# Optimization experiments

Measured on AMD Instinct MI355X. Metric: run time of the kernel, lower is better.

Reference implementation:

```python
import jax, jax.numpy as jnp
import numpy as np

D_MODEL = 512
NHEAD = 8
HEAD_DIM = D_MODEL // NHEAD
A, B = 1024, 16


def setup_inputs() -> dict:
    key = jax.random.key(0)
    ks = jax.random.split(key, 6)
    s = 1.0 / np.sqrt(D_MODEL)
    return {
        "src": jax.random.normal(ks[0], (A, B, D_MODEL), jnp.float32),
        "asset_relation_bias": jax.random.normal(ks[1], (A, A), jnp.float32) * 0.1,
        "Wq": jax.random.normal(ks[2], (D_MODEL, D_MODEL), jnp.float32) * s,
        "bq": jnp.zeros((D_MODEL,), jnp.float32),
        "Wk": jax.random.normal(ks[3], (D_MODEL, D_MODEL), jnp.float32) * s,
        "bk": jnp.zeros((D_MODEL,), jnp.float32),
        "Wv": jax.random.normal(ks[4], (D_MODEL, D_MODEL), jnp.float32) * s,
        "bv": jnp.zeros((D_MODEL,), jnp.float32),
        "Wo": jax.random.normal(ks[5], (D_MODEL, D_MODEL), jnp.float32) * s,
        "bo": jnp.zeros((D_MODEL,), jnp.float32),
    }


def reference(src, asset_relation_bias, Wq, bq, Wk, bk, Wv, bv, Wo, bo):
    # src: [A, B, H]; attention is over the asset dim A.
    scale = HEAD_DIM ** -0.5

    def proj_heads(x, W, b):
        y = x @ W.T + b                      # [A, B, H]  (torch Linear: x @ W.T + b)
        y = y.reshape(A, B, NHEAD, HEAD_DIM)
        return jnp.transpose(y, (1, 2, 0, 3))  # [B, nh, A, hd]

    q = proj_heads(src, Wq, bq)
    k = proj_heads(src, Wk, bk)
    v = proj_heads(src, Wv, bv)

    logits = jnp.einsum("bnad,bnkd->bnak", q, k) * scale  # [B, nh, A, A]
    logits = logits + asset_relation_bias[None, None]     # additive relation bias
    attn = jax.nn.softmax(logits, axis=-1)                # dropout = identity (eval)
    out = jnp.einsum("bnak,bnkd->bnad", attn, v)          # [B, nh, A, hd]
    out = jnp.transpose(out, (2, 0, 1, 3)).reshape(A, B, D_MODEL)
    out = out @ Wo.T + bo
    return out
```

## Files before the change

kernel.cpp:

```cpp
#include <hip/hip_runtime.h>
#include <hip/hip_bf16.h>

#define A_DIM 1024
#define B_DIM 16
#define DM    512
#define NH    8
#define HD    64

#define LDT 72

typedef short s16x8 __attribute__((ext_vector_type(8)));
typedef float f32x4 __attribute__((ext_vector_type(4)));

static __device__ __forceinline__ unsigned short f2b(float f) {
    __hip_bfloat16 h = __float2bfloat16(f);
    unsigned short u;
    __builtin_memcpy(&u, &h, 2);
    return u;
}
static __device__ __forceinline__ uint2 cvt4(float4 v) {
    __hip_bfloat162 lo = __float22bfloat162_rn(make_float2(v.x, v.y));
    __hip_bfloat162 hi = __float22bfloat162_rn(make_float2(v.z, v.w));
    unsigned int ulo, uhi;
    __builtin_memcpy(&ulo, &lo, 4);
    __builtin_memcpy(&uhi, &hi, 4);
    return make_uint2(ulo, uhi);
}

__global__ __launch_bounds__(256) void cvt_src(
    const float* __restrict__ in, short* __restrict__ out)
{
    int i = (blockIdx.x * 256 + threadIdx.x) * 8;
    float4 a = *(const float4*)&in[i];
    float4 b = *(const float4*)&in[i + 4];
    *(uint2*)&out[i]     = cvt4(a);
    *(uint2*)&out[i + 4] = cvt4(b);
}

__global__ __launch_bounds__(256) void cvt_w(
    const float* __restrict__ Wq, const float* __restrict__ Wk,
    const float* __restrict__ Wv, const float* __restrict__ Wo,
    short* __restrict__ Wall)
{
    int i = blockIdx.x * 256 + threadIdx.x;
    int mat = i >> 15;
    const float* W = (mat == 0) ? Wq : (mat == 1) ? Wk : (mat == 2) ? Wv : Wo;
    int j = (i & 32767) * 8;
    float4 a = *(const float4*)&W[j];
    float4 b = *(const float4*)&W[j + 4];
    *(uint2*)&Wall[mat * (DM * DM) + j]     = cvt4(a);
    *(uint2*)&Wall[mat * (DM * DM) + j + 4] = cvt4(b);
}

__global__ __launch_bounds__(256) void qkv_gemm_bf(
    const short* __restrict__ Sb, const short* __restrict__ Wall,
    const float* __restrict__ bq, const float* __restrict__ bk,
    const float* __restrict__ bv,
    short* __restrict__ Qb, short* __restrict__ Kb, short* __restrict__ Vb)
{
    __shared__ short As[128 * LDT];
    __shared__ short Bs[128 * LDT];

    const int tid  = threadIdx.x;
    const int wave = tid >> 6, lane = tid & 63;
    const int quad = lane >> 4, l16 = lane & 15;
    const int waveM = (wave >> 1) * 64, waveN = (wave & 1) * 64;
    const int mbase = blockIdx.y * 128;
    const int nbase = blockIdx.x * 128;
    const int mat   = nbase >> 9;
    const short* Wm   = Wall + mat * (DM * DM);
    const float* bvec = (mat == 0) ? bq : (mat == 1) ? bk : bv;
    short* dst        = (mat == 0) ? Qb : (mat == 1) ? Kb : Vb;
    const float oscale = (mat == 0) ? 0.125f : 1.0f;
    const int wrow0 = nbase & 511;

    f32x4 acc[4][4];
    #pragma unroll
    for (int i = 0; i < 4; i++)
        #pragma unroll
        for (int j = 0; j < 4; j++)
            acc[i][j] = (f32x4){0.f, 0.f, 0.f, 0.f};

    for (int kb = 0; kb < 8; ++kb) {
        __syncthreads();
        #pragma unroll
        for (int p = 0; p < 4; p++) {
            int chunk = tid + p * 256;
            int row = chunk >> 3, c = chunk & 7;
            *(s16x8*)&As[row * LDT + c * 8] =
                *(const s16x8*)&Sb[(mbase + row) * 512 + kb * 64 + c * 8];
            *(s16x8*)&Bs[row * LDT + c * 8] =
                *(const s16x8*)&Wm[(wrow0 + row) * 512 + kb * 64 + c * 8];
        }
        __syncthreads();
        #pragma unroll
        for (int k0i = 0; k0i < 2; k0i++) {
            s16x8 af[4], bf[4];
            #pragma unroll
            for (int mi = 0; mi < 4; mi++)
                af[mi] = *(const s16x8*)&As[(waveM + mi * 16 + l16) * LDT + (k0i * 4 + quad) * 8];
            #pragma unroll
            for (int ni = 0; ni < 4; ni++)
                bf[ni] = *(const s16x8*)&Bs[(waveN + ni * 16 + l16) * LDT + (k0i * 4 + quad) * 8];
            #pragma unroll
            for (int mi = 0; mi < 4; mi++)
                #pragma unroll
                for (int ni = 0; ni < 4; ni++)
                    acc[mi][ni] = __builtin_amdgcn_mfma_f32_16x16x32_bf16(
                        af[mi], bf[ni], acc[mi][ni], 0, 0, 0);
        }
    }

    #pragma unroll
    for (int mi = 0; mi < 4; mi++) {
        #pragma unroll
        for (int ni = 0; ni < 4; ni++) {
            #pragma unroll
            for (int r = 0; r < 4; r++) {
                int t = mbase + waveM + mi * 16 + quad * 4 + r;
                int o = wrow0 + waveN + ni * 16 + l16;
                float v = (acc[mi][ni][r] + bvec[o]) * oscale;
                int a = t >> 4, bb = t & 15, n = o >> 6, d = o & 63;
                dst[((bb * NH + n) * A_DIM + a) * HD + d] = (short)f2b(v);
            }
        }
    }
}

__global__ __launch_bounds__(256) void qkv_gemm(
    const float* __restrict__ src,
    const float* __restrict__ Wq, const float* __restrict__ bq,
    const float* __restrict__ Wk, const float* __restrict__ bk,
    const float* __restrict__ Wv, const float* __restrict__ bv,
    short* __restrict__ Qb, short* __restrict__ Kb, short* __restrict__ Vb)
{
    __shared__ short As[128 * LDT];
    __shared__ short Bs[128 * LDT];

    const int tid  = threadIdx.x;
    const int wave = tid >> 6, lane = tid & 63;
    const int quad = lane >> 4, l16 = lane & 15;
    const int waveM = (wave >> 1) * 64, waveN = (wave & 1) * 64;
    const int mbase = blockIdx.y * 128;
    const int nbase = blockIdx.x * 128;
    const int mat   = nbase >> 9;
    const float* W    = (mat == 0) ? Wq : (mat == 1) ? Wk : Wv;
    const float* bvec = (mat == 0) ? bq : (mat == 1) ? bk : bv;
    short* dst        = (mat == 0) ? Qb : (mat == 1) ? Kb : Vb;
    const float oscale = (mat == 0) ? 0.125f : 1.0f;
    const int wrow0 = nbase & 511;

    f32x4 acc[4][4];
    #pragma unroll
    for (int i = 0; i < 4; i++)
        #pragma unroll
        for (int j = 0; j < 4; j++)
            acc[i][j] = (f32x4){0.f, 0.f, 0.f, 0.f};

    for (int kb = 0; kb < 8; ++kb) {
        __syncthreads();
        #pragma unroll
        for (int p = 0; p < 8; p++) {
            int chunk = tid + p * 256;
            int row = chunk >> 4, c = chunk & 15;
            float4 a4 = *(const float4*)&src[(mbase + row) * 512 + kb * 64 + c * 4];
            *(uint2*)&As[row * LDT + c * 4] = cvt4(a4);
            float4 w4 = *(const float4*)&W[(wrow0 + row) * 512 + kb * 64 + c * 4];
            *(uint2*)&Bs[row * LDT + c * 4] = cvt4(w4);
        }
        __syncthreads();
        #pragma unroll
        for (int k0i = 0; k0i < 2; k0i++) {
            s16x8 af[4], bf[4];
            #pragma unroll
            for (int mi = 0; mi < 4; mi++)
                af[mi] = *(const s16x8*)&As[(waveM + mi * 16 + l16) * LDT + (k0i * 4 + quad) * 8];
            #pragma unroll
            for (int ni = 0; ni < 4; ni++)
                bf[ni] = *(const s16x8*)&Bs[(waveN + ni * 16 + l16) * LDT + (k0i * 4 + quad) * 8];
            #pragma unroll
            for (int mi = 0; mi < 4; mi++)
                #pragma unroll
                for (int ni = 0; ni < 4; ni++)
                    acc[mi][ni] = __builtin_amdgcn_mfma_f32_16x16x32_bf16(
                        af[mi], bf[ni], acc[mi][ni], 0, 0, 0);
        }
    }

    #pragma unroll
    for (int mi = 0; mi < 4; mi++) {
        #pragma unroll
        for (int ni = 0; ni < 4; ni++) {
            #pragma unroll
            for (int r = 0; r < 4; r++) {
                int t = mbase + waveM + mi * 16 + quad * 4 + r;
                int o = wrow0 + waveN + ni * 16 + l16;
                float v = (acc[mi][ni][r] + bvec[o]) * oscale;
                int a = t >> 4, bb = t & 15, n = o >> 6, d = o & 63;
                dst[((bb * NH + n) * A_DIM + a) * HD + d] = (short)f2b(v);
            }
        }
    }
}

__global__ __launch_bounds__(256) void attn_kernel(
    const short* __restrict__ Qb, const short* __restrict__ Kb,
    const short* __restrict__ Vb, const float* __restrict__ bias,
    short* __restrict__ AO)
{
    __shared__ short Ks[64 * LDT];
    __shared__ short Vt[64 * LDT];
    __shared__ short Ps[4][16 * LDT];

    const int tid  = threadIdx.x;
    const int wave = tid >> 6, lane = tid & 63;
    const int quad = lane >> 4, l16 = lane & 15;
    const int bn = blockIdx.y;
    const int qrow0 = blockIdx.x * 64 + wave * 16;

    const short* Qg = Qb + bn * (A_DIM * HD);
    const short* Kg = Kb + bn * (A_DIM * HD);
    const short* Vg = Vb + bn * (A_DIM * HD);

    s16x8 qf[2];
    #pragma unroll
    for (int k0i = 0; k0i < 2; k0i++)
        qf[k0i] = *(const s16x8*)&Qg[(qrow0 + l16) * HD + k0i * 32 + quad * 8];

    float lsum[4];
    f32x4 of[4];
    #pragma unroll
    for (int r = 0; r < 4; r++) lsum[r] = 0.f;
    #pragma unroll
    for (int db = 0; db < 4; db++) of[db] = (f32x4){0.f, 0.f, 0.f, 0.f};

    for (int kb = 0; kb < 16; ++kb) {
        __syncthreads();
        #pragma unroll
        for (int p = 0; p < 2; p++) {
            int chunk = tid + p * 256;
            int row = chunk >> 3, c = chunk & 7;
            *(s16x8*)&Ks[row * LDT + c * 8] =
                *(const s16x8*)&Kg[(kb * 64 + row) * HD + c * 8];
            s16x8 vv = *(const s16x8*)&Vg[(kb * 64 + row) * HD + c * 8];
            #pragma unroll
            for (int j = 0; j < 8; j++) {
                int d = c * 8 + j;
                Vt[d * LDT + (((row >> 3) ^ c) << 3) + (row & 7)] = vv[j];
            }
        }
        __syncthreads();

        float sv[4][4];
        #pragma unroll
        for (int cb = 0; cb < 4; cb++) {
            f32x4 s = (f32x4){0.f, 0.f, 0.f, 0.f};
            #pragma unroll
            for (int k0i = 0; k0i < 2; k0i++) {
                s16x8 kf = *(const s16x8*)&Ks[(cb * 16 + l16) * LDT + (k0i * 4 + quad) * 8];
                s = __builtin_amdgcn_mfma_f32_16x16x32_bf16(qf[k0i], kf, s, 0, 0, 0);
            }
            #pragma unroll
            for (int r = 0; r < 4; r++) {
                int arow = qrow0 + quad * 4 + r;
                int kcol = kb * 64 + cb * 16 + l16;
                sv[cb][r] = s[r] + bias[arow * A_DIM + kcol];
            }
        }

        #pragma unroll
        for (int r = 0; r < 4; r++) {
            int prow = quad * 4 + r;
            #pragma unroll
            for (int cb = 0; cb < 4; cb++) {
                float pv = __expf(sv[cb][r]);
                lsum[r] += pv;
                Ps[wave][prow * LDT + cb * 16 + l16] = (short)f2b(pv);
            }
        }

        #pragma unroll
        for (int k0i = 0; k0i < 2; k0i++) {
            s16x8 pf = *(const s16x8*)&Ps[wave][l16 * LDT + (k0i * 4 + quad) * 8];
            #pragma unroll
            for (int db = 0; db < 4; db++) {
                int rr = db * 16 + l16;
                s16x8 vf = *(const s16x8*)&Vt[rr * LDT +
                            (((k0i * 4 + quad) ^ (rr >> 3)) << 3)];
                of[db] = __builtin_amdgcn_mfma_f32_16x16x32_bf16(pf, vf, of[db], 0, 0, 0);
            }
        }
    }

    #pragma unroll
    for (int r = 0; r < 4; r++) {
        float ps = lsum[r];
        ps += __shfl_xor(ps, 1);
        ps += __shfl_xor(ps, 2);
        ps += __shfl_xor(ps, 4);
        ps += __shfl_xor(ps, 8);
        lsum[r] = 1.0f / ps;
    }

    const int b = bn >> 3, n = bn & 7;
    #pragma unroll
    for (int db = 0; db < 4; db++) {
        #pragma unroll
        for (int r = 0; r < 4; r++) {
            int a = qrow0 + quad * 4 + r;
            int d = db * 16 + l16;
            float v = of[db][r] * lsum[r];
            AO[(a * B_DIM + b) * DM + n * HD + d] = (short)f2b(v);
        }
    }
}

__global__ __launch_bounds__(256) void out_gemm_bf(
    const short* __restrict__ Xin,
    const short* __restrict__ Wob, const float* __restrict__ bo,
    float* __restrict__ out)
{
    __shared__ short As[128 * LDT];
    __shared__ short Bs[128 * LDT];

    const int tid  = threadIdx.x;
    const int wave = tid >> 6, lane = tid & 63;
    const int quad = lane >> 4, l16 = lane & 15;
    const int waveM = (wave >> 1) * 64, waveN = (wave & 1) * 64;
    const int mbase = blockIdx.y * 128;
    const int nbase = blockIdx.x * 128;

    f32x4 acc[4][4];
    #pragma unroll
    for (int i = 0; i < 4; i++)
        #pragma unroll
        for (int j = 0; j < 4; j++)
            acc[i][j] = (f32x4){0.f, 0.f, 0.f, 0.f};

    for (int kb = 0; kb < 8; ++kb) {
        __syncthreads();
        #pragma unroll
        for (int p = 0; p < 4; p++) {
            int chunk = tid + p * 256;
            int row = chunk >> 3, c = chunk & 7;
            *(s16x8*)&As[row * LDT + c * 8] =
                *(const s16x8*)&Xin[(mbase + row) * 512 + kb * 64 + c * 8];
            *(s16x8*)&Bs[row * LDT + c * 8] =
                *(const s16x8*)&Wob[(nbase + row) * 512 + kb * 64 + c * 8];
        }
        __syncthreads();
        #pragma unroll
        for (int k0i = 0; k0i < 2; k0i++) {
            s16x8 af[4], bf[4];
            #pragma unroll
            for (int mi = 0; mi < 4; mi++)
                af[mi] = *(const s16x8*)&As[(waveM + mi * 16 + l16) * LDT + (k0i * 4 + quad) * 8];
            #pragma unroll
            for (int ni = 0; ni < 4; ni++)
                bf[ni] = *(const s16x8*)&Bs[(waveN + ni * 16 + l16) * LDT + (k0i * 4 + quad) * 8];
            #pragma unroll
            for (int mi = 0; mi < 4; mi++)
                #pragma unroll
                for (int ni = 0; ni < 4; ni++)
                    acc[mi][ni] = __builtin_amdgcn_mfma_f32_16x16x32_bf16(
                        af[mi], bf[ni], acc[mi][ni], 0, 0, 0);
        }
    }

    #pragma unroll
    for (int mi = 0; mi < 4; mi++) {
        #pragma unroll
        for (int ni = 0; ni < 4; ni++) {
            #pragma unroll
            for (int r = 0; r < 4; r++) {
                int t = mbase + waveM + mi * 16 + quad * 4 + r;
                int o = nbase + waveN + ni * 16 + l16;
                out[t * 512 + o] = acc[mi][ni][r] + bo[o];
            }
        }
    }
}

__global__ __launch_bounds__(256) void out_gemm(
    const short* __restrict__ Xin,
    const float* __restrict__ Wo, const float* __restrict__ bo,
    float* __restrict__ out)
{
    __shared__ short As[128 * LDT];
    __shared__ short Bs[128 * LDT];

    const int tid  = threadIdx.x;
    const int wave = tid >> 6, lane = tid & 63;
    const int quad = lane >> 4, l16 = lane & 15;
    const int waveM = (wave >> 1) * 64, waveN = (wave & 1) * 64;
    const int mbase = blockIdx.y * 128;
    const int nbase = blockIdx.x * 128;

    f32x4 acc[4][4];
    #pragma unroll
    for (int i = 0; i < 4; i++)
        #pragma unroll
        for (int j = 0; j < 4; j++)
            acc[i][j] = (f32x4){0.f, 0.f, 0.f, 0.f};

    for (int kb = 0; kb < 8; ++kb) {
        __syncthreads();
        #pragma unroll
        for (int p = 0; p < 4; p++) {
            int chunk = tid + p * 256;
            int row = chunk >> 3, c = chunk & 7;
            *(s16x8*)&As[row * LDT + c * 8] =
                *(const s16x8*)&Xin[(mbase + row) * 512 + kb * 64 + c * 8];
        }
        #pragma unroll
        for (int p = 0; p < 8; p++) {
            int chunk = tid + p * 256;
            int row = chunk >> 4, c = chunk & 15;
            float4 w4 = *(const float4*)&Wo[(nbase + row) * 512 + kb * 64 + c * 4];
            *(uint2*)&Bs[row * LDT + c * 4] = cvt4(w4);
        }
        __syncthreads();
        #pragma unroll
        for (int k0i = 0; k0i < 2; k0i++) {
            s16x8 af[4], bf[4];
            #pragma unroll
            for (int mi = 0; mi < 4; mi++)
                af[mi] = *(const s16x8*)&As[(waveM + mi * 16 + l16) * LDT + (k0i * 4 + quad) * 8];
            #pragma unroll
            for (int ni = 0; ni < 4; ni++)
                bf[ni] = *(const s16x8*)&Bs[(waveN + ni * 16 + l16) * LDT + (k0i * 4 + quad) * 8];
            #pragma unroll
            for (int mi = 0; mi < 4; mi++)
                #pragma unroll
                for (int ni = 0; ni < 4; ni++)
                    acc[mi][ni] = __builtin_amdgcn_mfma_f32_16x16x32_bf16(
                        af[mi], bf[ni], acc[mi][ni], 0, 0, 0);
        }
    }

    #pragma unroll
    for (int mi = 0; mi < 4; mi++) {
        #pragma unroll
        for (int ni = 0; ni < 4; ni++) {
            #pragma unroll
            for (int r = 0; r < 4; r++) {
                int t = mbase + waveM + mi * 16 + quad * 4 + r;
                int o = nbase + waveN + ni * 16 + l16;
                out[t * 512 + o] = acc[mi][ni][r] + bo[o];
            }
        }
    }
}

extern "C" void kernel_launch(void* const* d_in, const int* in_sizes, int n_in,
                              void* d_out, int out_size, void* d_ws, size_t ws_size,
                              hipStream_t stream) {
    const float* src  = (const float*)d_in[0];
    const float* bias = (const float*)d_in[1];
    const float* Wq   = (const float*)d_in[2];
    const float* bq   = (const float*)d_in[3];
    const float* Wk   = (const float*)d_in[4];
    const float* bk   = (const float*)d_in[5];
    const float* Wv   = (const float*)d_in[6];
    const float* bv   = (const float*)d_in[7];
    const float* Wo   = (const float*)d_in[8];
    const float* bo   = (const float*)d_in[9];

    short* ws = (short*)d_ws;
    short* Qb = ws;
    short* Kb = ws + (size_t)(1 << 23);
    short* Vb = ws + (size_t)(2 << 23);

    const bool big2   = ws_size >= (size_t)(66u << 20);
    const bool big_ws = ws_size >= (size_t)(64u << 20);

    if (big2) {
        short* Sb   = ws + (size_t)3 * (1 << 23);
        short* Wall = ws + (size_t)4 * (1 << 23);
        short* AO   = Sb;

        cvt_src<<<dim3(4096), 256, 0, stream>>>(src, Sb);
        cvt_w<<<dim3(512), 256, 0, stream>>>(Wq, Wk, Wv, Wo, Wall);
        qkv_gemm_bf<<<dim3(12, 128), 256, 0, stream>>>(Sb, Wall, bq, bk, bv, Qb, Kb, Vb);
        attn_kernel<<<dim3(16, 128), 256, 0, stream>>>(Qb, Kb, Vb, bias, AO);
        out_gemm_bf<<<dim3(4, 128), 256, 0, stream>>>(AO, Wall + 3 * (DM * DM), bo,
                                                      (float*)d_out);
    } else {
        short* AO = big_ws ? (ws + (size_t)3 * (1 << 23))
                           : (short*)d_out;

        qkv_gemm<<<dim3(12, 128), 256, 0, stream>>>(src, Wq, bq, Wk, bk, Wv, bv, Qb, Kb, Vb);
        attn_kernel<<<dim3(16, 128), 256, 0, stream>>>(Qb, Kb, Vb, bias, AO);

        if (big_ws) {
            out_gemm<<<dim3(4, 128), 256, 0, stream>>>(AO, Wo, bo, (float*)d_out);
        } else {
            float* Cs = (float*)d_ws;
            out_gemm<<<dim3(4, 128), 256, 0, stream>>>(AO, Wo, bo, Cs);
            (void)hipMemcpyAsync(d_out, Cs, (size_t)out_size * sizeof(float),
                                 hipMemcpyDeviceToDevice, stream);
        }
    }
}
```

Before: 241.6 us.

## Use direct global-to-LDS loads with XOR-swizzled tiles in projection GEMMs

Replaces the register-staged global-to-shared copies in the QKV and output projection GEMMs with global_load_lds 16-byte direct loads into LDS. The padded LDT=72 layout becomes an unpadded 64-wide tile with an XOR swizzle on the 8-element column chunk, which keeps fragment reads free of bank conflicts. The aim is to cut VGPR traffic and instruction count in the tile-load phase. It depends on the hardware supporting 16-byte LDS-direct loads, and the attention kernel, which likely dominates runtime, is untouched.

Result: no change. 241.8 us (+0.1%).

```diff
diff --git a/kernel.cpp b/kernel.cpp
--- a/kernel.cpp
+++ b/kernel.cpp
@@ -25,6 +25,12 @@
     __builtin_memcpy(&ulo, &lo, 4);
     __builtin_memcpy(&uhi, &hi, 4);
     return make_uint2(ulo, uhi);
+}
+
+static __device__ __forceinline__ void gl_lds16(const short* g, short* l) {
+    __builtin_amdgcn_global_load_lds(
+        (const __attribute__((address_space(1))) unsigned int*)g,
+        (__attribute__((address_space(3))) unsigned int*)l, 16, 0, 0);
 }
 
 __global__ __launch_bounds__(256) void cvt_src(
@@ -58,8 +64,8 @@
     const float* __restrict__ bv,
     short* __restrict__ Qb, short* __restrict__ Kb, short* __restrict__ Vb)
 {
-    __shared__ short As[128 * LDT];
-    __shared__ short Bs[128 * LDT];
+    __shared__ __align__(16) short As[128 * 64];
+    __shared__ __align__(16) short Bs[128 * 64];
 
     const int tid  = threadIdx.x;
     const int wave = tid >> 6, lane = tid & 63;
@@ -74,6 +80,10 @@
     const float oscale = (mat == 0) ? 0.125f : 1.0f;
     const int wrow0 = nbase & 511;
 
+    const int srow = lane >> 3;
+    const int scol = (lane & 7) ^ srow;
+    const int cxa  = l16 & 7;
+
     f32x4 acc[4][4];
     #pragma unroll
     for (int i = 0; i < 4; i++)
@@ -85,12 +95,12 @@
         __syncthreads();
         #pragma unroll
         for (int p = 0; p < 4; p++) {
-            int chunk = tid + p * 256;
-            int row = chunk >> 3, c = chunk & 7;
-            *(s16x8*)&As[row * LDT + c * 8] =
-                *(const s16x8*)&Sb[(mbase + row) * 512 + kb * 64 + c * 8];
-            *(s16x8*)&Bs[row * LDT + c * 8] =
-                *(const s16x8*)&Wm[(wrow0 + row) * 512 + kb * 64 + c * 8];
+            int ch = wave + p * 4;
+            int r  = ch * 8 + srow;
+            gl_lds16(&Sb[(mbase + r) * 512 + kb * 64 + scol * 8],
+                     &As[ch * 8 * 64]);
+            gl_lds16(&Wm[(wrow0 + r) * 512 + kb * 64 + scol * 8],
+                     &Bs[ch * 8 * 64]);
         }
         __syncthreads();
         #pragma unroll
@@ -98,10 +108,12 @@
             s16x8 af[4], bf[4];
             #pragma unroll
             for (int mi = 0; mi < 4; mi++)
-                af[mi] = *(const s16x8*)&As[(waveM + mi * 16 + l16) * LDT + (k0i * 4 + quad) * 8];
+                af[mi] = *(const s16x8*)&As[(waveM + mi * 16 + l16) * 64
+                                            + (((k0i * 4 + quad) ^ cxa) * 8)];
             #pragma unroll
             for (int ni = 0; ni < 4; ni++)
-                bf[ni] = *(const s16x8*)&Bs[(waveN + ni * 16 + l16) * LDT + (k0i * 4 + quad) * 8];
+                bf[ni] = *(const s16x8*)&Bs[(waveN + ni * 16 + l16) * 64
+                                            + (((k0i * 4 + quad) ^ cxa) * 8)];
             #pragma unroll
             for (int mi = 0; mi < 4; mi++)
                 #pragma unroll
@@ -320,8 +332,8 @@
     const short* __restrict__ Wob, const float* __restrict__ bo,
     float* __restrict__ out)
 {
-    __shared__ short As[128 * LDT];
-    __shared__ short Bs[128 * LDT];
+    __shared__ __align__(16) short As[128 * 64];
+    __shared__ __align__(16) short Bs[128 * 64];
 
     const int tid  = threadIdx.x;
     const int wave = tid >> 6, lane = tid & 63;
@@ -330,6 +342,10 @@
     const int mbase = blockIdx.y * 128;
     const int nbase = blockIdx.x * 128;
 
+    const int srow = lane >> 3;
+    const int scol = (lane & 7) ^ srow;
+    const int cxa  = l16 & 7;
+
     f32x4 acc[4][4];
     #pragma unroll
     for (int i = 0; i < 4; i++)
@@ -341,12 +357,12 @@
         __syncthreads();
         #pragma unroll
         for (int p = 0; p < 4; p++) {
-            int chunk = tid + p * 256;
-            int row = chunk >> 3, c = chunk & 7;
-            *(s16x8*)&As[row * LDT + c * 8] =
-                *(const s16x8*)&Xin[(mbase + row) * 512 + kb * 64 + c * 8];
-            *(s16x8*)&Bs[row * LDT + c * 8] =
-                *(const s16x8*)&Wob[(nbase + row) * 512 + kb * 64 + c * 8];
+            int ch = wave + p * 4;
+            int r  = ch * 8 + srow;
+            gl_lds16(&Xin[(mbase + r) * 512 + kb * 64 + scol * 8],
+                     &As[ch * 8 * 64]);
+            gl_lds16(&Wob[(nbase + r) * 512 + kb * 64 + scol * 8],
+                     &Bs[ch * 8 * 64]);
         }
         __syncthreads();
         #pragma unroll
@@ -354,10 +370,12 @@
             s16x8 af[4], bf[4];
             #pragma unroll
             for (int mi = 0; mi < 4; mi++)
-                af[mi] = *(const s16x8*)&As[(waveM + mi * 16 + l16) * LDT + (k0i * 4 + quad) * 8];
+                af[mi] = *(const s16x8*)&As[(waveM + mi * 16 + l16) * 64
+                                            + (((k0i * 4 + quad) ^ cxa) * 8)];
             #pragma unroll
             for (int ni = 0; ni < 4; ni++)
-                bf[ni] = *(const s16x8*)&Bs[(waveN + ni * 16 + l16) * LDT + (k0i * 4 + quad) * 8];
+                bf[ni] = *(const s16x8*)&Bs[(waveN + ni * 16 + l16) * 64
+                                            + (((k0i * 4 + quad) ^ cxa) * 8)];
             #pragma unroll
             for (int mi = 0; mi < 4; mi++)
                 #pragma unroll
```
